# Optimization experiments

Hardware: AMD Instinct MI355X
Metric: run time of the kernel (lower is better)

The kernel has to match this reference:

```python
import jax, jax.numpy as jnp
import numpy as np

B, N_LATENT, H, N_GENES, G_OI, K = 512, 64, 32, 20000, 5000, 64
BN_EPS = 1e-5


def setup_inputs() -> dict:
    key = jax.random.key(0)
    ks = jax.random.split(key, 8)
    latent = jax.random.normal(ks[0], (B, N_LATENT), dtype=jnp.float32)
    genes_oi = jax.random.randint(ks[1], (G_OI,), 0, N_GENES, dtype=jnp.int64)
    # MLP layer (n_layers=1): Linear(n_latent, H) + ReLU + BatchNorm1d(H) (eval) + Dropout (eval = identity)
    W1 = jax.random.normal(ks[2], (N_LATENT, H), dtype=jnp.float32) / np.sqrt(N_LATENT)
    b1 = jnp.zeros((H,), dtype=jnp.float32)
    bn_gamma = jnp.ones((H,), dtype=jnp.float32)
    bn_beta = jnp.zeros((H,), dtype=jnp.float32)
    bn_mean = jnp.zeros((H,), dtype=jnp.float32)
    bn_var = jnp.ones((H,), dtype=jnp.float32)
    # per-gene embedding tensors, init like the torch module
    stdv_logit = 1.0 / np.sqrt(H)
    logit_weight = jax.random.uniform(ks[3], (N_GENES, H, K), dtype=jnp.float32,
                                      minval=-stdv_logit, maxval=stdv_logit)
    stdv_rho = 1.0 / np.sqrt(H) / 100.0
    rho_weight = jax.random.uniform(ks[4], (N_GENES, H), dtype=jnp.float32,
                                    minval=-stdv_rho, maxval=stdv_rho)
    return {"latent": latent, "genes_oi": genes_oi, "W1": W1, "b1": b1,
            "bn_gamma": bn_gamma, "bn_beta": bn_beta, "bn_mean": bn_mean,
            "bn_var": bn_var, "logit_weight": logit_weight, "rho_weight": rho_weight}


def reference(latent, genes_oi, W1, b1, bn_gamma, bn_beta, bn_mean, bn_var,
              logit_weight, rho_weight):
    # shared MLP: Linear -> ReLU -> BatchNorm1d(eval) -> Dropout(eval=identity)
    h = jax.nn.relu(latent @ W1 + b1)                                  # [B, H]
    h = bn_gamma * (h - bn_mean) * jax.lax.rsqrt(bn_var + BN_EPS) + bn_beta
    # gather per-gene weights
    lw = logit_weight[genes_oi]                                        # [G, H, K]
    rw = rho_weight[genes_oi]                                          # [G, H]
    # [B,1,1,H] @ [G,H,K] -> [B,G,1,K] -> squeeze(-2) -> [B,G,K]
    logit = jnp.einsum("bh,ghk->bgk", h, lw)
    # [B,H] @ [H,G] -> [B,G]
    rho = jnp.einsum("bh,gh->bg", h, rw)
    return logit, rho
```

## Files before the change

kernel.cpp:

```cpp
#include <hip/hip_runtime.h>
#include <hip/hip_bf16.h>
#include <cstdint>

#define B_SZ   512
#define NLAT   64
#define H_SZ   32
#define G_OI_N 5000
#define K_SZ   64

#define GPC    8
#define NCHUNK 625

typedef __attribute__((ext_vector_type(8))) short short8v;
typedef __attribute__((ext_vector_type(4))) float float4v;

__device__ __forceinline__ unsigned short f2bf(float x) {
    union { float f; unsigned u; } v; v.f = x;
    unsigned r = v.u + 0x7fff + ((v.u >> 16) & 1);
    return (unsigned short)(r >> 16);
}

__global__ __launch_bounds__(256) void mlp_kernel(
    const float* __restrict__ latent, const float* __restrict__ W1,
    const float* __restrict__ b1, const float* __restrict__ gamma,
    const float* __restrict__ beta, const float* __restrict__ mean,
    const float* __restrict__ var, float* __restrict__ hout,
    unsigned short* __restrict__ hbf)
{
    int idx = blockIdx.x * 256 + threadIdx.x;
    int b = idx >> 5;
    int j = idx & 31;
    float acc = 0.f;
    const float4* lp = reinterpret_cast<const float4*>(latent + b * NLAT);
#pragma unroll
    for (int q = 0; q < NLAT / 4; ++q) {
        float4 lv = lp[q];
        acc = fmaf(lv.x, W1[(4 * q + 0) * H_SZ + j], acc);
        acc = fmaf(lv.y, W1[(4 * q + 1) * H_SZ + j], acc);
        acc = fmaf(lv.z, W1[(4 * q + 2) * H_SZ + j], acc);
        acc = fmaf(lv.w, W1[(4 * q + 3) * H_SZ + j], acc);
    }
    acc += b1[j];
    acc = fmaxf(acc, 0.f);
    acc = gamma[j] * (acc - mean[j]) * rsqrtf(var[j] + 1e-5f) + beta[j];
    hout[idx] = acc;
    hbf[idx]  = f2bf(acc);
}

__global__ __launch_bounds__(256) void logit_kernel(
    const unsigned short* __restrict__ hbf, const int* __restrict__ genes,
    const float* __restrict__ lw, float* __restrict__ out)
{
    const int bh    = blockIdx.x & 1;
    const int chunk = blockIdx.x >> 1;
    const int lane  = threadIdx.x & 63;
    const int kt    = threadIdx.x >> 6;
    const int row16 = lane & 15;
    const int kg    = lane >> 4;
    const int b0    = bh * 256;

    short8v hfr[16];
#pragma unroll
    for (int mt = 0; mt < 16; ++mt)
        hfr[mt] = *reinterpret_cast<const short8v*>(
            hbf + (b0 + mt * 16 + row16) * H_SZ + kg * 8);

    const int g0 = chunk * GPC;
    short8v afr[GPC];
#pragma unroll
    for (int gi = 0; gi < GPC; ++gi) {
        const size_t gene = (size_t)genes[g0 + gi];
        const float* ap = lw + gene * (size_t)(H_SZ * K_SZ)
                             + (size_t)(kg * 8) * K_SZ + kt * 16 + row16;
#pragma unroll
        for (int j = 0; j < 8; ++j)
            afr[gi][j] = (short)f2bf(ap[(size_t)j * K_SZ]);
    }

    const size_t GK = (size_t)G_OI_N * K_SZ;
    float* orow = out + (size_t)g0 * K_SZ + kt * 16 + kg * 4;
    for (int mt = 0; mt < 16; ++mt) {
        float* obase = orow + (size_t)(b0 + mt * 16 + row16) * GK;
#pragma unroll
        for (int gi = 0; gi < GPC; ++gi) {
            float4v acc = {0.f, 0.f, 0.f, 0.f};
            acc = __builtin_amdgcn_mfma_f32_16x16x32_bf16(afr[gi], hfr[mt], acc, 0, 0, 0);
            *reinterpret_cast<float4v*>(obase + (size_t)gi * K_SZ) = acc;
        }
    }
}

__global__ __launch_bounds__(256) void rho_kernel(
    const float* __restrict__ hbuf, const int* __restrict__ genes,
    const float* __restrict__ rw, float* __restrict__ out)
{
    const int gx = blockIdx.x % 20;
    const int bx = blockIdx.x / 20;
    const int g = gx * 256 + threadIdx.x;
    if (g >= G_OI_N) return;
    const size_t gene = (size_t)genes[g];

    float rreg[H_SZ];
    const float4* rp = reinterpret_cast<const float4*>(rw + gene * H_SZ);
#pragma unroll
    for (int q = 0; q < 8; ++q) {
        float4 rv = rp[q];
        rreg[4 * q + 0] = rv.x; rreg[4 * q + 1] = rv.y;
        rreg[4 * q + 2] = rv.z; rreg[4 * q + 3] = rv.w;
    }

    const int b0 = bx * 32;
    for (int b = b0; b < b0 + 32; ++b) {
        const float4* hp = reinterpret_cast<const float4*>(hbuf + b * H_SZ);
        float a0 = 0.f, a1 = 0.f, a2 = 0.f, a3 = 0.f;
#pragma unroll
        for (int q = 0; q < 8; ++q) {
            float4 hv = hp[q];
            a0 = fmaf(hv.x, rreg[4 * q + 0], a0);
            a1 = fmaf(hv.y, rreg[4 * q + 1], a1);
            a2 = fmaf(hv.z, rreg[4 * q + 2], a2);
            a3 = fmaf(hv.w, rreg[4 * q + 3], a3);
        }
        out[(size_t)b * G_OI_N + g] = (a0 + a1) + (a2 + a3);
    }
}

extern "C" void kernel_launch(void* const* d_in, const int* in_sizes, int n_in,
                              void* d_out, int out_size, void* d_ws, size_t ws_size,
                              hipStream_t stream)
{
    const float *latent = nullptr, *W1 = nullptr, *lw = nullptr, *rw = nullptr;
    const int* genes = nullptr;
    const float* small[5] = {nullptr, nullptr, nullptr, nullptr, nullptr};
    int nsmall = 0;
    for (int i = 0; i < n_in; ++i) {
        switch (in_sizes[i]) {
            case 32768:    latent = (const float*)d_in[i]; break;
            case 5000:
            case 10000:    genes  = (const int*)d_in[i];   break;
            case 2048:     W1     = (const float*)d_in[i]; break;
            case 40960000: lw     = (const float*)d_in[i]; break;
            case 640000:   rw     = (const float*)d_in[i]; break;
            case 32: if (nsmall < 5) small[nsmall++] = (const float*)d_in[i]; break;
            default: break;
        }
    }
    if (!latent || !genes || !W1 || !lw || !rw || nsmall < 5) return;
    const float* b1v   = small[0];
    const float* gamma = small[1];
    const float* beta  = small[2];
    const float* mean  = small[3];
    const float* var   = small[4];

    float* hbuf = (float*)d_ws;
    unsigned short* hbf = (unsigned short*)((char*)d_ws + 65536);
    float* logit_out = (float*)d_out;
    float* rho_out   = logit_out + (size_t)B_SZ * G_OI_N * K_SZ;

    mlp_kernel<<<(B_SZ * H_SZ) / 256, 256, 0, stream>>>(latent, W1, b1v, gamma, beta,
                                                        mean, var, hbuf, hbf);
    logit_kernel<<<2 * NCHUNK, 256, 0, stream>>>(hbf, genes, lw, logit_out);
    rho_kernel<<<20 * 16, 256, 0, stream>>>(hbuf, genes, rw, rho_out);
}
```

Measured before the change: 178.6 us.

## Stage logit tiles through padded LDS for contiguous output stores, widen gene chunk

The logit kernel now writes MFMA results into a padded shared-memory tile, then copies them out so each row's stores cover 10 consecutive genes (640 contiguous floats) instead of scattered 16-byte fragments. The gene chunk grows from 8 to 20 and the batch is split into four quarters instead of two, which changes the grid shape and how much of h each block holds in registers. In exchange it adds two block barriers per half-tile and LDS traffic, and raises register pressure from holding 20 weight fragments per thread.

```diff
diff --git a/kernel.cpp b/kernel.cpp
--- a/kernel.cpp
+++ b/kernel.cpp
@@ -8,8 +8,9 @@
 #define G_OI_N 5000
 #define K_SZ   64
 
-#define GPC    8
-#define NCHUNK 625
+#define GPC    20
+#define NCHUNK 250
+#define KPAD   68
 
 typedef __attribute__((ext_vector_type(8))) short short8v;
 typedef __attribute__((ext_vector_type(4))) float float4v;
@@ -51,17 +52,19 @@
     const unsigned short* __restrict__ hbf, const int* __restrict__ genes,
     const float* __restrict__ lw, float* __restrict__ out)
 {
-    const int bh    = blockIdx.x & 1;
-    const int chunk = blockIdx.x >> 1;
-    const int lane  = threadIdx.x & 63;
-    const int kt    = threadIdx.x >> 6;
+    __shared__ float lt[16 * 10 * KPAD];
+    const int bq    = blockIdx.x & 3;
+    const int chunk = blockIdx.x >> 2;
+    const int tid   = threadIdx.x;
+    const int lane  = tid & 63;
+    const int kt    = tid >> 6;
     const int row16 = lane & 15;
     const int kg    = lane >> 4;
-    const int b0    = bh * 256;
+    const int b0    = bq * 128;
 
-    short8v hfr[16];
+    short8v hfr[8];
 #pragma unroll
-    for (int mt = 0; mt < 16; ++mt)
+    for (int mt = 0; mt < 8; ++mt)
         hfr[mt] = *reinterpret_cast<const short8v*>(
             hbf + (b0 + mt * 16 + row16) * H_SZ + kg * 8);
 
@@ -78,14 +81,33 @@
     }
 
     const size_t GK = (size_t)G_OI_N * K_SZ;
-    float* orow = out + (size_t)g0 * K_SZ + kt * 16 + kg * 4;
-    for (int mt = 0; mt < 16; ++mt) {
-        float* obase = orow + (size_t)(b0 + mt * 16 + row16) * GK;
+    for (int mt = 0; mt < 8; ++mt) {
 #pragma unroll
-        for (int gi = 0; gi < GPC; ++gi) {
-            float4v acc = {0.f, 0.f, 0.f, 0.f};
-            acc = __builtin_amdgcn_mfma_f32_16x16x32_bf16(afr[gi], hfr[mt], acc, 0, 0, 0);
-            *reinterpret_cast<float4v*>(obase + (size_t)gi * K_SZ) = acc;
+        for (int half = 0; half < 2; ++half) {
+#pragma unroll
+            for (int gi = 0; gi < 10; ++gi) {
+                float4v acc = {0.f, 0.f, 0.f, 0.f};
+                acc = __builtin_amdgcn_mfma_f32_16x16x32_bf16(
+                          afr[half * 10 + gi], hfr[mt], acc, 0, 0, 0);
+                *reinterpret_cast<float4v*>(
+                    lt + row16 * (10 * KPAD) + gi * KPAD + kt * 16 + kg * 4) = acc;
+            }
+            __syncthreads();
+            float* obase = out + (size_t)(g0 + half * 10) * K_SZ
+                               + (size_t)(b0 + mt * 16) * GK;
+#pragma unroll
+            for (int p = 0; p < 10; ++p) {
+                const int f   = p * 256 + tid;
+                const int r   = f / 160;
+                const int rem = f - r * 160;
+                const int g   = rem >> 4;
+                const int k4  = rem & 15;
+                float4v v = *reinterpret_cast<const float4v*>(
+                    lt + r * (10 * KPAD) + g * KPAD + k4 * 4);
+                *reinterpret_cast<float4v*>(
+                    obase + (size_t)r * GK + g * K_SZ + k4 * 4) = v;
+            }
+            __syncthreads();
         }
     }
 }
@@ -159,6 +181,6 @@
 
     mlp_kernel<<<(B_SZ * H_SZ) / 256, 256, 0, stream>>>(latent, W1, b1v, gamma, beta,
                                                         mean, var, hbuf, hbf);
-    logit_kernel<<<2 * NCHUNK, 256, 0, stream>>>(hbf, genes, lw, logit_out);
+    logit_kernel<<<4 * NCHUNK, 256, 0, stream>>>(hbf, genes, lw, logit_out);
     rho_kernel<<<20 * 16, 256, 0, stream>>>(hbuf, genes, rw, rho_out);
 }
```

Result: slower. 187.4 us (+4.9%).

## Split logit work across waves by batch rows instead of K tiles

Applied to the files above, without the earlier changes.

Each wave now owns 64 batch rows and all four K tiles, where before it owned one K tile across all 256 rows. Every wave loads the full gene weight fragments (4x more gathered loads per wave, converted to bf16) and only 4 h fragments. Each thread then writes a contiguous 256-byte output row segment per gene, aiming for better store coalescing on the dominant 655MB output write. The cost is redundant weight loads across the four waves and higher register use from afr[8][4].

```diff
diff --git a/kernel.cpp b/kernel.cpp
--- a/kernel.cpp
+++ b/kernel.cpp
@@ -54,38 +54,47 @@
     const int bh    = blockIdx.x & 1;
     const int chunk = blockIdx.x >> 1;
     const int lane  = threadIdx.x & 63;
-    const int kt    = threadIdx.x >> 6;
+    const int w     = threadIdx.x >> 6;
     const int row16 = lane & 15;
     const int kg    = lane >> 4;
-    const int b0    = bh * 256;
+    const int b0w   = bh * 256 + w * 64;
 
-    short8v hfr[16];
+    short8v hfr[4];
 #pragma unroll
-    for (int mt = 0; mt < 16; ++mt)
-        hfr[mt] = *reinterpret_cast<const short8v*>(
-            hbf + (b0 + mt * 16 + row16) * H_SZ + kg * 8);
+    for (int m = 0; m < 4; ++m)
+        hfr[m] = *reinterpret_cast<const short8v*>(
+            hbf + (b0w + m * 16 + row16) * H_SZ + kg * 8);
 
     const int g0 = chunk * GPC;
-    short8v afr[GPC];
+    short8v afr[GPC][4];
 #pragma unroll
     for (int gi = 0; gi < GPC; ++gi) {
         const size_t gene = (size_t)genes[g0 + gi];
-        const float* ap = lw + gene * (size_t)(H_SZ * K_SZ)
-                             + (size_t)(kg * 8) * K_SZ + kt * 16 + row16;
+        const float* ap = lw + gene * (size_t)(H_SZ * K_SZ) + kg * 512 + row16;
 #pragma unroll
-        for (int j = 0; j < 8; ++j)
-            afr[gi][j] = (short)f2bf(ap[(size_t)j * K_SZ]);
+        for (int kt = 0; kt < 4; ++kt)
+#pragma unroll
+            for (int j = 0; j < 8; ++j)
+                afr[gi][kt][j] = (short)f2bf(ap[kt * 16 + (size_t)j * K_SZ]);
     }
 
     const size_t GK = (size_t)G_OI_N * K_SZ;
-    float* orow = out + (size_t)g0 * K_SZ + kt * 16 + kg * 4;
-    for (int mt = 0; mt < 16; ++mt) {
-        float* obase = orow + (size_t)(b0 + mt * 16 + row16) * GK;
+#pragma unroll
+    for (int m = 0; m < 4; ++m) {
 #pragma unroll
         for (int gi = 0; gi < GPC; ++gi) {
-            float4v acc = {0.f, 0.f, 0.f, 0.f};
-            acc = __builtin_amdgcn_mfma_f32_16x16x32_bf16(afr[gi], hfr[mt], acc, 0, 0, 0);
-            *reinterpret_cast<float4v*>(obase + (size_t)gi * K_SZ) = acc;
+            float* obase = out + (size_t)(g0 + gi) * K_SZ
+                         + (size_t)(b0w + m * 16 + row16) * GK + kg * 4;
+            float4v a0 = {0.f,0.f,0.f,0.f}, a1 = {0.f,0.f,0.f,0.f};
+            float4v a2 = {0.f,0.f,0.f,0.f}, a3 = {0.f,0.f,0.f,0.f};
+            a0 = __builtin_amdgcn_mfma_f32_16x16x32_bf16(afr[gi][0], hfr[m], a0, 0, 0, 0);
+            a1 = __builtin_amdgcn_mfma_f32_16x16x32_bf16(afr[gi][1], hfr[m], a1, 0, 0, 0);
+            a2 = __builtin_amdgcn_mfma_f32_16x16x32_bf16(afr[gi][2], hfr[m], a2, 0, 0, 0);
+            a3 = __builtin_amdgcn_mfma_f32_16x16x32_bf16(afr[gi][3], hfr[m], a3, 0, 0, 0);
+            *reinterpret_cast<float4v*>(obase +  0) = a0;
+            *reinterpret_cast<float4v*>(obase + 16) = a1;
+            *reinterpret_cast<float4v*>(obase + 32) = a2;
+            *reinterpret_cast<float4v*>(obase + 48) = a3;
         }
     }
 }
```

Measured after the change: 205.2 us, median of 3. 14.9% more time.

## Give each wave one gene and stage MFMA output through LDS for coalesced stores

Applied to the files above, without the earlier changes.

Each wave now owns a single gene and computes all four K tiles for it, instead of each wave owning one K tile across eight genes. The MFMA results go into a per-wave XOR-swizzled shared-memory tile and are read back so that each row store covers a full contiguous 256-byte K row. Previously each store wrote scattered 16-byte pieces. The change adds an LDS round trip and doubles the grid to 2500 blocks, and it relies on 16 KB of LDS per block.

```diff
diff --git a/kernel.cpp b/kernel.cpp
--- a/kernel.cpp
+++ b/kernel.cpp
@@ -8,8 +8,7 @@
 #define G_OI_N 5000
 #define K_SZ   64
 
-#define GPC    8
-#define NCHUNK 625
+#define NCHUNK 1250
 
 typedef __attribute__((ext_vector_type(8))) short short8v;
 typedef __attribute__((ext_vector_type(4))) float float4v;
@@ -51,13 +50,29 @@
     const unsigned short* __restrict__ hbf, const int* __restrict__ genes,
     const float* __restrict__ lw, float* __restrict__ out)
 {
+    __shared__ float lt[4 * 1024];
     const int bh    = blockIdx.x & 1;
     const int chunk = blockIdx.x >> 1;
     const int lane  = threadIdx.x & 63;
-    const int kt    = threadIdx.x >> 6;
+    const int w     = threadIdx.x >> 6;
     const int row16 = lane & 15;
     const int kg    = lane >> 4;
     const int b0    = bh * 256;
+    char* wt = reinterpret_cast<char*>(lt + w * 1024);
+
+    const int g = chunk * 4 + w;
+    const size_t gene = (size_t)genes[g];
+
+    short8v afr[4];
+    {
+        const float* ap = lw + gene * (size_t)(H_SZ * K_SZ)
+                             + (size_t)(kg * 8) * K_SZ + row16;
+#pragma unroll
+        for (int kt = 0; kt < 4; ++kt)
+#pragma unroll
+            for (int j = 0; j < 8; ++j)
+                afr[kt][j] = (short)f2bf(ap[kt * 16 + (size_t)j * K_SZ]);
+    }
 
     short8v hfr[16];
 #pragma unroll
@@ -65,27 +80,25 @@
         hfr[mt] = *reinterpret_cast<const short8v*>(
             hbf + (b0 + mt * 16 + row16) * H_SZ + kg * 8);
 
-    const int g0 = chunk * GPC;
-    short8v afr[GPC];
+    const size_t GK = (size_t)G_OI_N * K_SZ;
+    float* og = out + (size_t)g * K_SZ;
+    for (int mt = 0; mt < 16; ++mt) {
 #pragma unroll
-    for (int gi = 0; gi < GPC; ++gi) {
-        const size_t gene = (size_t)genes[g0 + gi];
-        const float* ap = lw + gene * (size_t)(H_SZ * K_SZ)
-                             + (size_t)(kg * 8) * K_SZ + kt * 16 + row16;
+        for (int kt = 0; kt < 4; ++kt) {
+            float4v acc = {0.f, 0.f, 0.f, 0.f};
+            acc = __builtin_amdgcn_mfma_f32_16x16x32_bf16(afr[kt], hfr[mt], acc, 0, 0, 0);
+            int off = row16 * 256 + kt * 64 + kg * 16;
+            off ^= (row16 & 7) << 4;
+            *reinterpret_cast<float4v*>(wt + off) = acc;
+        }
 #pragma unroll
-        for (int j = 0; j < 8; ++j)
-            afr[gi][j] = (short)f2bf(ap[(size_t)j * K_SZ]);
-    }
-
-    const size_t GK = (size_t)G_OI_N * K_SZ;
-    float* orow = out + (size_t)g0 * K_SZ + kt * 16 + kg * 4;
-    for (int mt = 0; mt < 16; ++mt) {
-        float* obase = orow + (size_t)(b0 + mt * 16 + row16) * GK;
-#pragma unroll
-        for (int gi = 0; gi < GPC; ++gi) {
-            float4v acc = {0.f, 0.f, 0.f, 0.f};
-            acc = __builtin_amdgcn_mfma_f32_16x16x32_bf16(afr[gi], hfr[mt], acc, 0, 0, 0);
-            *reinterpret_cast<float4v*>(obase + (size_t)gi * K_SZ) = acc;
+        for (int r2 = 0; r2 < 4; ++r2) {
+            const int rrow = 4 * r2 + kg;
+            int roff = rrow * 256 + row16 * 16;
+            roff ^= (rrow & 7) << 4;
+            float4v v = *reinterpret_cast<const float4v*>(wt + roff);
+            *reinterpret_cast<float4v*>(
+                og + (size_t)(b0 + mt * 16 + rrow) * GK + row16 * 4) = v;
         }
     }
 }
```

After: 163.0 us. 8.8% less time.
